# Kernel optimization log

Measured on AMD Instinct MI355X. Metric: run time of the kernel, lower is better.

The kernel has to match this reference:

```python
import jax, jax.numpy as jnp
import numpy as np

N_NODES = 100000
N_EDGES = 3200000
N_FEATS = 512
HIDDEN = 16
N_CLASSES = 40


def gcn_conv(x, edge_index, W, b):
    """PyG-style GCNConv: linear -> symmetric-normalized scatter-add -> bias."""
    n = x.shape[0]
    src, dst = edge_index[0], edge_index[1]
    # add self-loops
    loop = jnp.arange(n, dtype=src.dtype)
    src = jnp.concatenate([src, loop])
    dst = jnp.concatenate([dst, loop])
    # symmetric normalization deg^{-1/2}[src] * deg^{-1/2}[dst]
    deg = jax.ops.segment_sum(jnp.ones_like(src, dtype=x.dtype), dst, num_segments=n)
    dinv = jnp.where(deg > 0, jax.lax.rsqrt(jnp.maximum(deg, 1.0)), 0.0)
    norm = dinv[src] * dinv[dst]  # [E+N]
    h = x @ W                     # [N, out]
    msg = h[src] * norm[:, None]  # gather + scale, [E+N, out]
    out = jax.ops.segment_sum(msg, dst, num_segments=n)  # scatter-add at targets
    return out + b


def setup_inputs() -> dict:
    key = jax.random.key(0)
    k1, k2, k3, k4 = jax.random.split(key, 4)
    x = jax.random.normal(k1, (N_NODES, N_FEATS), dtype=jnp.float32)
    edge_index = jax.random.randint(k2, (2, N_EDGES), 0, N_NODES, dtype=jnp.int64)
    # Glorot-ish scaled weights
    W1 = jax.random.normal(k3, (N_FEATS, HIDDEN), dtype=jnp.float32) * (1.0 / np.sqrt(N_FEATS))
    b1 = jnp.zeros((HIDDEN,), dtype=jnp.float32)
    W2 = jax.random.normal(k4, (HIDDEN, N_CLASSES), dtype=jnp.float32) * (1.0 / np.sqrt(HIDDEN))
    b2 = jnp.zeros((N_CLASSES,), dtype=jnp.float32)
    return {"x": x, "edge_index": edge_index, "W1": W1, "b1": b1, "W2": W2, "b2": b2}


def reference(x, edge_index, W1, b1, W2, b2):
    h = gcn_conv(x, edge_index, W1, b1)
    h = jax.nn.relu(h)
    # dropout is identity in eval mode
    h = gcn_conv(h, edge_index, W2, b2)
    return jax.nn.log_softmax(h, axis=1)
```

## Files before the change

kernel.cpp:

```cpp
#include <hip/hip_runtime.h>
#include <hip/hip_bf16.h>

#define NN 100000
#define NE 3200000
#define NF 512
#define NH 16
#define NC 40
#define BKT_SH 6
#define NBKT 1563
#define CAP2 2560
#define NBLK 512
#define CHUNK 6250
#define GEMMB 1563

typedef __attribute__((ext_vector_type(4))) float f32x4;
typedef __attribute__((ext_vector_type(8))) short bf16x8;

static __device__ __forceinline__ unsigned short f2b(float f) {
    unsigned int u = __float_as_uint(f);
    u += 0x7FFFu + ((u >> 16) & 1u);
    return (unsigned short)(u >> 16);
}
static __device__ __forceinline__ float b2f(unsigned short u) {
    return __uint_as_float(((unsigned int)u) << 16);
}


__global__ void __launch_bounds__(256) kA_gemm_hist(const float* __restrict__ x,
                                                    const float* __restrict__ W1,
                                                    const int* __restrict__ ei,
                                                    unsigned short* __restrict__ h1,
                                                    int* __restrict__ histG) {
    __shared__ int smem[4096];
    int tid = threadIdx.x;
    if (blockIdx.x < NBLK) {
        int* h = smem;
        for (int i = tid; i < NBKT; i += 256) h[i] = 0;
        __syncthreads();
        int b = blockIdx.x;
        int e0 = b * CHUNK, e1 = min(NE, e0 + CHUNK);
        for (int e = e0 + tid; e < e1; e += 256)
            atomicAdd(&h[((unsigned)ei[NE + e]) >> BKT_SH], 1);
        __syncthreads();
        for (int i = tid; i < NBKT; i += 256)
            histG[b * NBKT + i] = h[i];
        __syncthreads();
    }
    unsigned short* wl = (unsigned short*)smem;
    for (int idx = tid; idx < 8192; idx += 256) {
        int s = idx >> 9;
        int l = (idx >> 3) & 63;
        int e = idx & 7;
        int k = s * 32 + (l >> 4) * 8 + e;
        wl[idx] = f2b(W1[k * 16 + (l & 15)]);
    }
    __syncthreads();
    int wave = tid >> 6;
    int l = tid & 63;
    int m0 = blockIdx.x * 64 + wave * 16;
    if (m0 >= NN) return;
    int row = m0 + (l & 15);
    int krow = (l >> 4) * 8;
    const float* xr = x + (size_t)row * NF + krow;
    const unsigned short* wf = wl + l * 8;
    f32x4 acc = {0.f, 0.f, 0.f, 0.f};
#pragma unroll 4
    for (int s = 0; s < 16; ++s) {
        f32x4 xa = *(const f32x4*)(xr + s * 32);
        f32x4 xb = *(const f32x4*)(xr + s * 32 + 4);
        union { bf16x8 v; unsigned short u[8]; } a;
        a.u[0] = f2b(xa.x); a.u[1] = f2b(xa.y); a.u[2] = f2b(xa.z); a.u[3] = f2b(xa.w);
        a.u[4] = f2b(xb.x); a.u[5] = f2b(xb.y); a.u[6] = f2b(xb.z); a.u[7] = f2b(xb.w);
        bf16x8 b = *(const bf16x8*)(wf + s * 512);
        acc = __builtin_amdgcn_mfma_f32_16x16x32_bf16(a.v, b, acc, 0, 0, 0);
    }
#pragma unroll
    for (int r = 0; r < 4; ++r) {
        int orow = m0 + (l >> 4) * 4 + r;
        h1[(size_t)orow * NH + (l & 15)] = f2b(acc[r]);
    }
}


__global__ void __launch_bounds__(512) k_colscan(const int* __restrict__ histG,
                                                 int* __restrict__ ofsG,
                                                 int* __restrict__ bcnt) {
    __shared__ int sh[NBLK];
    int k = blockIdx.x;
    int t = threadIdx.x;
    int v = histG[t * NBKT + k];
    sh[t] = v;
    __syncthreads();
    for (int off = 1; off < NBLK; off <<= 1) {
        int add = (t >= off) ? sh[t - off] : 0;
        __syncthreads();
        sh[t] += add;
        __syncthreads();
    }
    ofsG[k * NBLK + t] = sh[t] - v;
    if (t == NBLK - 1) bcnt[k] = sh[t];
}


__global__ void k_bscan(const int* __restrict__ bcnt, int* __restrict__ bptr,
                        int* __restrict__ rowptr) {
    __shared__ int sh[1024];
    int t = threadIdx.x;
    int i0 = 2 * t, i1 = 2 * t + 1;
    int a = (i0 < NBKT) ? bcnt[i0] : 0;
    int b = (i1 < NBKT) ? bcnt[i1] : 0;
    int pair = a + b;
    sh[t] = pair;
    __syncthreads();
    for (int off = 1; off < 1024; off <<= 1) {
        int add = (t >= off) ? sh[t - off] : 0;
        __syncthreads();
        sh[t] += add;
        __syncthreads();
    }
    int excl = sh[t] - pair;
    if (i0 < NBKT) bptr[i0] = excl;
    if (i1 < NBKT) bptr[i1] = excl + a;
    if (t == 0) { bptr[NBKT] = NE; rowptr[NN] = NE; }
}


__global__ void __launch_bounds__(512) k_msscatter(const int* __restrict__ ei,
                                                   const int* __restrict__ bptr,
                                                   const int* __restrict__ ofsG,
                                                   unsigned int* __restrict__ pairs) {
    __shared__ int lcur[NBKT];
    int b = blockIdx.x;
    for (int k = threadIdx.x; k < NBKT; k += 512)
        lcur[k] = bptr[k] + ofsG[k * NBLK + b];
    __syncthreads();
    int e0 = b * CHUNK, e1 = min(NE, e0 + CHUNK);
    for (int e = e0 + threadIdx.x; e < e1; e += 512) {
        unsigned int s = (unsigned int)ei[e];
        unsigned int d = (unsigned int)ei[NE + e];
        int pos = atomicAdd(&lcur[d >> BKT_SH], 1);
        pairs[pos] = s | ((d & 63u) << 17);
    }
}


__global__ void __launch_bounds__(256) k_bsort(const unsigned int* __restrict__ pairs,
                                               const int* __restrict__ bptr,
                                               int* __restrict__ rowptr,
                                               float* __restrict__ dinv,
                                               int* __restrict__ ssrc) {
    __shared__ unsigned int ein[CAP2];
    __shared__ unsigned int srt[CAP2];
    __shared__ int lcnt[64], lofs[64], lcur[64];
    int b = blockIdx.x;
    int s0 = bptr[b], s1 = bptr[b + 1];
    int n = s1 - s0;
    for (int i = threadIdx.x; i < n; i += 256) ein[i] = pairs[s0 + i];
    if (threadIdx.x < 64) lcnt[threadIdx.x] = 0;
    __syncthreads();
    for (int i = threadIdx.x; i < n; i += 256) atomicAdd(&lcnt[ein[i] >> 17], 1);
    __syncthreads();
    if (threadIdx.x < 64) lofs[threadIdx.x] = lcnt[threadIdx.x];
    __syncthreads();
    for (int off = 1; off < 64; off <<= 1) {
        int add = 0;
        if (threadIdx.x < 64 && threadIdx.x >= off) add = lofs[threadIdx.x - off];
        __syncthreads();
        if (threadIdx.x < 64) lofs[threadIdx.x] += add;
        __syncthreads();
    }
    if (threadIdx.x < 64) {
        int excl = lofs[threadIdx.x] - lcnt[threadIdx.x];
        lcur[threadIdx.x] = excl;
        int node = b * 64 + threadIdx.x;
        if (node < NN) {
            rowptr[node] = s0 + excl;
            dinv[node] = rsqrtf((float)(lcnt[threadIdx.x] + 1));
        }
    }
    __syncthreads();
    for (int i = threadIdx.x; i < n; i += 256) {
        unsigned int v = ein[i];
        int pos = atomicAdd(&lcur[v >> 17], 1);
        srt[pos] = v & 0x1FFFFu;
    }
    __syncthreads();
    for (int i = threadIdx.x; i < n; i += 256) ssrc[s0 + i] = (int)srt[i];
}


__global__ void __launch_bounds__(256) k_agg1(const unsigned short* __restrict__ hs,
                                              const int* __restrict__ rowptr,
                                              const int* __restrict__ ssrc,
                                              const float* __restrict__ dinv,
                                              const float* __restrict__ b1,
                                              unsigned short* __restrict__ r1) {
    int l = threadIdx.x & 63;
    int node = blockIdx.x * 4 + (threadIdx.x >> 6);
    int j = l & 15;
    int ec = l >> 4;
    float di = dinv[node];
    int s = rowptr[node];
    int e1 = rowptr[node + 1];
    float acc = (ec == 0) ? b2f(hs[(size_t)node * NH + j]) * di : 0.0f;
#pragma unroll 4
    for (int e = s + ec; e < e1; e += 4) {
        int src = ssrc[e];
        acc += b2f(hs[(size_t)src * NH + j]) * dinv[src];
    }
    acc += __shfl_xor(acc, 16, 64);
    acc += __shfl_xor(acc, 32, 64);
    if (ec == 0) {
        float o = fmaxf(acc * di + b1[j], 0.0f) * di;
        r1[(size_t)node * NH + j] = f2b(o);
    }
}


__global__ void __launch_bounds__(256) k_agg2(const unsigned short* __restrict__ rs,
                                              const int* __restrict__ rowptr,
                                              const int* __restrict__ ssrc,
                                              const float* __restrict__ dinv,
                                              const float* __restrict__ W2,
                                              const float* __restrict__ b2,
                                              float* __restrict__ out) {
    __shared__ float w[NH * NC];
    __shared__ float bb[NC];
    int t = threadIdx.x;
    for (int i = t; i < NH * NC; i += 256) w[i] = W2[i];
    if (t < NC) bb[t] = b2[t];
    __syncthreads();
    int l = t & 63;
    int node = blockIdx.x * 4 + (t >> 6);
    int j = l & 15;
    int ec = l >> 4;
    float di = dinv[node];
    int s = rowptr[node];
    int e1 = rowptr[node + 1];
    float acc = (ec == 0) ? b2f(rs[(size_t)node * NH + j]) : 0.0f;
#pragma unroll 4
    for (int e = s + ec; e < e1; e += 4) {
        int src = ssrc[e];
        acc += b2f(rs[(size_t)src * NH + j]);
    }
    acc += __shfl_xor(acc, 16, 64);
    acc += __shfl_xor(acc, 32, 64);
    float zv = acc * di;
    float lg = (l < NC) ? bb[l] : -1e30f;
#pragma unroll
    for (int k = 0; k < NH; ++k) {
        float zk = __shfl(zv, k, 64);
        if (l < NC) lg += zk * w[k * NC + l];
    }
    float mx = lg;
#pragma unroll
    for (int off = 1; off < 64; off <<= 1) mx = fmaxf(mx, __shfl_xor(mx, off, 64));
    float ex = (l < NC) ? __expf(lg - mx) : 0.0f;
    float sm = ex;
#pragma unroll
    for (int off = 1; off < 64; off <<= 1) sm += __shfl_xor(sm, off, 64);
    if (l < NC) out[(size_t)node * NC + l] = lg - mx - __logf(sm);
}


extern "C" void kernel_launch(void* const* d_in, const int* in_sizes, int n_in,
                              void* d_out, int out_size, void* d_ws, size_t ws_size,
                              hipStream_t stream) {
    const float* x  = (const float*)d_in[0];
    const int*   ei = (const int*)d_in[1];
    const float* W1 = (const float*)d_in[2];
    const float* b1 = (const float*)d_in[3];
    const float* W2 = (const float*)d_in[4];
    const float* b2 = (const float*)d_in[5];
    float* out = (float*)d_out;

    char* ws = (char*)d_ws;
    size_t off = 0;
    auto alloc = [&](size_t bytes) -> void* {
        void* p = ws + off;
        off += (bytes + 255) & ~(size_t)255;
        return p;
    };
    int* histG      = (int*)alloc((size_t)NBLK * NBKT * 4);
    int* ofsG       = (int*)alloc((size_t)NBKT * NBLK * 4);
    int* bcnt       = (int*)alloc((size_t)NBKT * 4);
    int* bptr       = (int*)alloc((size_t)(NBKT + 1) * 4);
    int* rowptr     = (int*)alloc((size_t)(NN + 1) * 4);
    float* dinv     = (float*)alloc((size_t)NN * 4);
    unsigned int* pairs = (unsigned int*)alloc((size_t)NE * 4);
    int* ssrc       = (int*)alloc((size_t)NE * 4);
    unsigned short* h1  = (unsigned short*)alloc((size_t)NN * NH * 2);
    unsigned short* r1  = (unsigned short*)alloc((size_t)NN * NH * 2);

    kA_gemm_hist<<<GEMMB, 256, 0, stream>>>(x, W1, ei, h1, histG);
    k_colscan<<<NBKT, NBLK, 0, stream>>>(histG, ofsG, bcnt);
    k_bscan<<<1, 1024, 0, stream>>>(bcnt, bptr, rowptr);
    k_msscatter<<<NBLK, 512, 0, stream>>>(ei, bptr, ofsG, pairs);
    k_bsort<<<NBKT, 256, 0, stream>>>(pairs, bptr, rowptr, dinv, ssrc);
    k_agg1<<<NN / 4, 256, 0, stream>>>(h1, rowptr, ssrc, dinv, b1, r1);
    k_agg2<<<NN / 4, 256, 0, stream>>>(r1, rowptr, ssrc, dinv, W2, b2, out);
}
```

Baseline: 255.3 us.

## Widen CSR buckets to 256 nodes and decouple histogram and scatter block counts

Bucket width for the two-level counting sort grows from 64 to 256 destination nodes, cutting the number of buckets from 1563 to 391. Histogramming now spreads over 1536 blocks (fused into the GEMM grid), while the scatter uses 256 blocks that each cover six histogram chunks, with the column scan summing triples. Fewer buckets shrink the offset tables and scan work, and bigger per-bucket local sorts use 1024-thread blocks. In exchange each local sort needs about 70KB of LDS for a bucket capped at 8960 edges, which lowers occupancy and would overflow if a bucket ever got larger.

```diff
diff --git a/kernel.cpp b/kernel.cpp
--- a/kernel.cpp
+++ b/kernel.cpp
@@ -6,11 +6,14 @@
 #define NF 512
 #define NH 16
 #define NC 40
-#define BKT_SH 6
-#define NBKT 1563
-#define CAP2 2560
-#define NBLK 512
-#define CHUNK 6250
+#define BKT_SH 8
+#define NBKT 391
+#define CAP 8960
+#define HISTB 1536
+#define CHUNK_H 2084
+#define SCATB 256
+#define ROWS_PER_SCAT 6
+#define CHUNK_S 12504
 #define GEMMB 1563
 
 typedef __attribute__((ext_vector_type(4))) float f32x4;
@@ -33,17 +36,17 @@
                                                     int* __restrict__ histG) {
     __shared__ int smem[4096];
     int tid = threadIdx.x;
-    if (blockIdx.x < NBLK) {
+    if (blockIdx.x < HISTB) {
         int* h = smem;
         for (int i = tid; i < NBKT; i += 256) h[i] = 0;
         __syncthreads();
-        int b = blockIdx.x;
-        int e0 = b * CHUNK, e1 = min(NE, e0 + CHUNK);
+        int r = blockIdx.x;
+        int e0 = r * CHUNK_H, e1 = min(NE, e0 + CHUNK_H);
         for (int e = e0 + tid; e < e1; e += 256)
             atomicAdd(&h[((unsigned)ei[NE + e]) >> BKT_SH], 1);
         __syncthreads();
         for (int i = tid; i < NBKT; i += 256)
-            histG[b * NBKT + i] = h[i];
+            histG[r * NBKT + i] = h[i];
         __syncthreads();
     }
     unsigned short* wl = (unsigned short*)smem;
@@ -85,107 +88,108 @@
 __global__ void __launch_bounds__(512) k_colscan(const int* __restrict__ histG,
                                                  int* __restrict__ ofsG,
                                                  int* __restrict__ bcnt) {
-    __shared__ int sh[NBLK];
+    __shared__ int sh[512];
     int k = blockIdx.x;
     int t = threadIdx.x;
-    int v = histG[t * NBKT + k];
-    sh[t] = v;
-    __syncthreads();
-    for (int off = 1; off < NBLK; off <<= 1) {
+    int base = t * 3;
+    int a0 = histG[(size_t)(base + 0) * NBKT + k];
+    int a1 = histG[(size_t)(base + 1) * NBKT + k];
+    int a2 = histG[(size_t)(base + 2) * NBKT + k];
+    int s = a0 + a1 + a2;
+    sh[t] = s;
+    __syncthreads();
+    for (int off = 1; off < 512; off <<= 1) {
         int add = (t >= off) ? sh[t - off] : 0;
         __syncthreads();
         sh[t] += add;
         __syncthreads();
     }
-    ofsG[k * NBLK + t] = sh[t] - v;
-    if (t == NBLK - 1) bcnt[k] = sh[t];
+    int excl = sh[t] - s;
+    if ((t & 1) == 0) ofsG[(size_t)k * SCATB + (t >> 1)] = excl;
+    if (t == 511) bcnt[k] = sh[t];
 }
 
 
 __global__ void k_bscan(const int* __restrict__ bcnt, int* __restrict__ bptr,
                         int* __restrict__ rowptr) {
-    __shared__ int sh[1024];
+    __shared__ int sh[512];
     int t = threadIdx.x;
-    int i0 = 2 * t, i1 = 2 * t + 1;
-    int a = (i0 < NBKT) ? bcnt[i0] : 0;
-    int b = (i1 < NBKT) ? bcnt[i1] : 0;
-    int pair = a + b;
-    sh[t] = pair;
-    __syncthreads();
-    for (int off = 1; off < 1024; off <<= 1) {
+    int v = (t < NBKT) ? bcnt[t] : 0;
+    sh[t] = v;
+    __syncthreads();
+    for (int off = 1; off < 512; off <<= 1) {
         int add = (t >= off) ? sh[t - off] : 0;
         __syncthreads();
         sh[t] += add;
         __syncthreads();
     }
-    int excl = sh[t] - pair;
-    if (i0 < NBKT) bptr[i0] = excl;
-    if (i1 < NBKT) bptr[i1] = excl + a;
+    if (t < NBKT) bptr[t] = sh[t] - v;
     if (t == 0) { bptr[NBKT] = NE; rowptr[NN] = NE; }
 }
 
 
-__global__ void __launch_bounds__(512) k_msscatter(const int* __restrict__ ei,
-                                                   const int* __restrict__ bptr,
-                                                   const int* __restrict__ ofsG,
-                                                   unsigned int* __restrict__ pairs) {
+__global__ void __launch_bounds__(1024) k_msscatter(const int* __restrict__ ei,
+                                                    const int* __restrict__ bptr,
+                                                    const int* __restrict__ ofsG,
+                                                    unsigned int* __restrict__ pairs) {
     __shared__ int lcur[NBKT];
     int b = blockIdx.x;
-    for (int k = threadIdx.x; k < NBKT; k += 512)
-        lcur[k] = bptr[k] + ofsG[k * NBLK + b];
-    __syncthreads();
-    int e0 = b * CHUNK, e1 = min(NE, e0 + CHUNK);
-    for (int e = e0 + threadIdx.x; e < e1; e += 512) {
+    for (int k = threadIdx.x; k < NBKT; k += 1024)
+        lcur[k] = bptr[k] + ofsG[(size_t)k * SCATB + b];
+    __syncthreads();
+    int e0 = b * CHUNK_S, e1 = min(NE, e0 + CHUNK_S);
+    for (int e = e0 + threadIdx.x; e < e1; e += 1024) {
         unsigned int s = (unsigned int)ei[e];
         unsigned int d = (unsigned int)ei[NE + e];
         int pos = atomicAdd(&lcur[d >> BKT_SH], 1);
-        pairs[pos] = s | ((d & 63u) << 17);
-    }
-}
-
-
-__global__ void __launch_bounds__(256) k_bsort(const unsigned int* __restrict__ pairs,
-                                               const int* __restrict__ bptr,
-                                               int* __restrict__ rowptr,
-                                               float* __restrict__ dinv,
-                                               int* __restrict__ ssrc) {
-    __shared__ unsigned int ein[CAP2];
-    __shared__ unsigned int srt[CAP2];
-    __shared__ int lcnt[64], lofs[64], lcur[64];
+        pairs[pos] = s | ((d & 255u) << 17);
+    }
+}
+
+
+__global__ void __launch_bounds__(1024) k_bsort(const unsigned int* __restrict__ pairs,
+                                                const int* __restrict__ bptr,
+                                                int* __restrict__ rowptr,
+                                                float* __restrict__ dinv,
+                                                int* __restrict__ ssrc) {
+    __shared__ unsigned int ein[CAP];
+    __shared__ unsigned int srt[CAP];
+    __shared__ int lcnt[256], lofs[256], lcur[256];
     int b = blockIdx.x;
+    int t = threadIdx.x;
     int s0 = bptr[b], s1 = bptr[b + 1];
     int n = s1 - s0;
-    for (int i = threadIdx.x; i < n; i += 256) ein[i] = pairs[s0 + i];
-    if (threadIdx.x < 64) lcnt[threadIdx.x] = 0;
-    __syncthreads();
-    for (int i = threadIdx.x; i < n; i += 256) atomicAdd(&lcnt[ein[i] >> 17], 1);
-    __syncthreads();
-    if (threadIdx.x < 64) lofs[threadIdx.x] = lcnt[threadIdx.x];
-    __syncthreads();
-    for (int off = 1; off < 64; off <<= 1) {
+    for (int i = t; i < n; i += 1024) ein[i] = pairs[s0 + i];
+    if (t < 256) lcnt[t] = 0;
+    __syncthreads();
+    for (int i = t; i < n; i += 1024) atomicAdd(&lcnt[ein[i] >> 17], 1);
+    __syncthreads();
+    if (t < 256) lofs[t] = lcnt[t];
+    __syncthreads();
+    for (int off = 1; off < 256; off <<= 1) {
         int add = 0;
-        if (threadIdx.x < 64 && threadIdx.x >= off) add = lofs[threadIdx.x - off];
-        __syncthreads();
-        if (threadIdx.x < 64) lofs[threadIdx.x] += add;
-        __syncthreads();
-    }
-    if (threadIdx.x < 64) {
-        int excl = lofs[threadIdx.x] - lcnt[threadIdx.x];
-        lcur[threadIdx.x] = excl;
-        int node = b * 64 + threadIdx.x;
+        if (t < 256 && t >= off) add = lofs[t - off];
+        __syncthreads();
+        if (t < 256) lofs[t] += add;
+        __syncthreads();
+    }
+    if (t < 256) {
+        int excl = lofs[t] - lcnt[t];
+        lcur[t] = excl;
+        int node = b * 256 + t;
         if (node < NN) {
             rowptr[node] = s0 + excl;
-            dinv[node] = rsqrtf((float)(lcnt[threadIdx.x] + 1));
+            dinv[node] = rsqrtf((float)(lcnt[t] + 1));
         }
     }
     __syncthreads();
-    for (int i = threadIdx.x; i < n; i += 256) {
+    for (int i = t; i < n; i += 1024) {
         unsigned int v = ein[i];
         int pos = atomicAdd(&lcur[v >> 17], 1);
         srt[pos] = v & 0x1FFFFu;
     }
     __syncthreads();
-    for (int i = threadIdx.x; i < n; i += 256) ssrc[s0 + i] = (int)srt[i];
+    for (int i = t; i < n; i += 1024) ssrc[s0 + i] = (int)srt[i];
 }
 
 
@@ -281,8 +285,8 @@
         off += (bytes + 255) & ~(size_t)255;
         return p;
     };
-    int* histG      = (int*)alloc((size_t)NBLK * NBKT * 4);
-    int* ofsG       = (int*)alloc((size_t)NBKT * NBLK * 4);
+    int* histG      = (int*)alloc((size_t)HISTB * NBKT * 4);
+    int* ofsG       = (int*)alloc((size_t)NBKT * SCATB * 4);
     int* bcnt       = (int*)alloc((size_t)NBKT * 4);
     int* bptr       = (int*)alloc((size_t)(NBKT + 1) * 4);
     int* rowptr     = (int*)alloc((size_t)(NN + 1) * 4);
@@ -293,10 +297,10 @@
     unsigned short* r1  = (unsigned short*)alloc((size_t)NN * NH * 2);
 
     kA_gemm_hist<<<GEMMB, 256, 0, stream>>>(x, W1, ei, h1, histG);
-    k_colscan<<<NBKT, NBLK, 0, stream>>>(histG, ofsG, bcnt);
-    k_bscan<<<1, 1024, 0, stream>>>(bcnt, bptr, rowptr);
-    k_msscatter<<<NBLK, 512, 0, stream>>>(ei, bptr, ofsG, pairs);
-    k_bsort<<<NBKT, 256, 0, stream>>>(pairs, bptr, rowptr, dinv, ssrc);
+    k_colscan<<<NBKT, 512, 0, stream>>>(histG, ofsG, bcnt);
+    k_bscan<<<1, 512, 0, stream>>>(bcnt, bptr, rowptr);
+    k_msscatter<<<SCATB, 1024, 0, stream>>>(ei, bptr, ofsG, pairs);
+    k_bsort<<<NBKT, 1024, 0, stream>>>(pairs, bptr, rowptr, dinv, ssrc);
     k_agg1<<<NN / 4, 256, 0, stream>>>(h1, rowptr, ssrc, dinv, b1, r1);
     k_agg2<<<NN / 4, 256, 0, stream>>>(r1, rowptr, ssrc, dinv, W2, b2, out);
 }
```

Measured after the change: 222.5 us. -12.9%, faster.
